# Performance work log

Measured on AMD Instinct MI355X. Metric: run time of the kernel, lower is better.

The kernel has to match this reference:

```python
import jax, jax.numpy as jnp
import numpy as np

ROPE_THETA = 10000.0

def rope(x):
    # RoPE over the FULL model_dim (applied pre head-split, as in the source),
    # interleaved even/odd pairs. x: [B, S, D]
    B, S, D = x.shape
    half = D // 2
    inv_freq = 1.0 / (ROPE_THETA ** (jnp.arange(half, dtype=jnp.float32) * 2.0 / D))
    ang = jnp.arange(S, dtype=jnp.float32)[:, None] * inv_freq[None, :]  # [S, half]
    cos, sin = jnp.cos(ang), jnp.sin(ang)
    x1, x2 = x[..., 0::2], x[..., 1::2]
    r1 = x1 * cos - x2 * sin
    r2 = x1 * sin + x2 * cos
    return jnp.stack([r1, r2], axis=-1).reshape(B, S, D)


def setup_inputs() -> dict:
    key = jax.random.key(0)
    ks = jax.random.split(key, 9)
    B, S, D = 4, 2048, 768
    w = 0.02
    return {
        "X":  jax.random.normal(ks[0], (B, S, D), dtype=jnp.float32),
        "Wq": jax.random.normal(ks[1], (D, D), dtype=jnp.float32) * w,
        "bq": jnp.zeros((D,), dtype=jnp.float32),
        "Wk": jax.random.normal(ks[2], (D, D), dtype=jnp.float32) * w,
        "bk": jnp.zeros((D,), dtype=jnp.float32),
        "Wv": jax.random.normal(ks[3], (D, D), dtype=jnp.float32) * w,
        "bv": jnp.zeros((D,), dtype=jnp.float32),
        "Wo": jax.random.normal(ks[4], (D, D), dtype=jnp.float32) * w,
        "bo": jnp.zeros((D,), dtype=jnp.float32),
    }


def reference(X, Wq, bq, Wk, bk, Wv, bv, Wo, bo):
    NUM_HEADS = 12
    B, S, D = X.shape
    hd = D // NUM_HEADS

    q = rope(X @ Wq + bq)   # RoPE applied pre-split on full model_dim
    k = rope(X @ Wk + bk)
    v = X @ Wv + bv

    # Contiguous per-head slices == reshape to [B, S, H, hd]
    qh = q.reshape(B, S, NUM_HEADS, hd)
    kh = k.reshape(B, S, NUM_HEADS, hd)
    vh = v.reshape(B, S, NUM_HEADS, hd)

    scores = jnp.einsum('bqhd,bkhd->bhqk', qh, kh) / jnp.sqrt(jnp.float32(hd))
    causal = jnp.tril(jnp.ones((S, S), dtype=bool))
    scores = jnp.where(causal[None, None, :, :], scores, -jnp.inf)
    weights = jax.nn.softmax(scores, axis=-1)
    out = jnp.einsum('bhqk,bkhd->bqhd', weights, vh).reshape(B, S, D)
    return out @ Wo + bo
```

## Files before the change

kernel.cpp:

```cpp
#include <hip/hip_runtime.h>
#include <math.h>

#define D_MODEL 768
#define NUM_HEADS 12
#define HEAD_DIM 64
#define SEQ 2048
#define BATCH 4
#define MROWS (BATCH * SEQ)
#define HALF_D (D_MODEL / 2)

typedef __bf16    bf16x8 __attribute__((ext_vector_type(8)));
typedef _Float16  f16x4  __attribute__((ext_vector_type(4)));
typedef float     f32x4  __attribute__((ext_vector_type(4)));

__device__ __forceinline__ void gload_lds16(const void* gp, void* lp) {
    __builtin_amdgcn_global_load_lds(
        (const __attribute__((address_space(1))) unsigned int*)gp,
        (__attribute__((address_space(3))) unsigned int*)lp, 16, 0, 0);
}

__global__ __launch_bounds__(256)
void prep(const float* __restrict__ X, __bf16* __restrict__ Xb,
          const float* __restrict__ W0, const float* __restrict__ W1,
          const float* __restrict__ W2, const float* __restrict__ W3,
          __bf16* __restrict__ T0, __bf16* __restrict__ T1,
          __bf16* __restrict__ T2, __bf16* __restrict__ T3)
{
    __shared__ float t[64][65];
    const int n   = blockIdx.x;
    const int tid = threadIdx.x;

    if (n < 3072) {
        size_t i = ((size_t)n * 256 + tid) * 8;
        float4 u = *(const float4*)(X + i);
        float4 v = *(const float4*)(X + i + 4);
        bf16x8 o;
        o[0]=(__bf16)u.x; o[1]=(__bf16)u.y; o[2]=(__bf16)u.z; o[3]=(__bf16)u.w;
        o[4]=(__bf16)v.x; o[5]=(__bf16)v.y; o[6]=(__bf16)v.z; o[7]=(__bf16)v.w;
        *(bf16x8*)(Xb + i) = o;
    } else {
        int m = n - 3072;
        int z = m / 144;
        int rem = m - z * 144;
        int by = rem / 12, bx = rem % 12;
        const float* W = z == 0 ? W0 : z == 1 ? W1 : z == 2 ? W2 : W3;
        __bf16*      T = z == 0 ? T0 : z == 1 ? T1 : z == 2 ? T2 : T3;

        const int r0 = by * 64, c0 = bx * 64;
        const int lx = tid & 63, g = tid >> 6;

        #pragma unroll
        for (int rr = 0; rr < 16; ++rr) {
            int r = g * 16 + rr;
            t[r][lx] = W[(size_t)(r0 + r) * D_MODEL + c0 + lx];
        }
        __syncthreads();

        const int nn = tid >> 2;
        const int kb = (tid & 3) * 16;
        bf16x8 o1, o2;
        #pragma unroll
        for (int mm = 0; mm < 8; ++mm) o1[mm] = (__bf16)t[kb + mm][nn];
        #pragma unroll
        for (int mm = 0; mm < 8; ++mm) o2[mm] = (__bf16)t[kb + 8 + mm][nn];
        __bf16* dst = T + (size_t)(c0 + nn) * D_MODEL + r0 + kb;
        *(bf16x8*)dst       = o1;
        *(bf16x8*)(dst + 8) = o2;
    }
}

__global__ __launch_bounds__(256)
void qkv_gemm(const __bf16* __restrict__ Xb,
              const __bf16* __restrict__ Wqt, const __bf16* __restrict__ Wkt,
              const __bf16* __restrict__ Wvt,
              const float* __restrict__ bq, const float* __restrict__ bk,
              const float* __restrict__ bv,
              __bf16* __restrict__ Qb, __bf16* __restrict__ Kb,
              _Float16* __restrict__ Vtb)
{
    __shared__ bf16x8 Asf[2][8][64];
    __shared__ bf16x8 Bsf[2][8][64];

    const int tid  = threadIdx.x;
    const int wv   = tid >> 6;
    const int ln   = tid & 63;
    const int t15  = ln & 15;
    const int quad = ln >> 4;
    const int wr = wv >> 1, wc = wv & 1;

    const int lin = blockIdx.x;
    const int c   = lin >> 6;
    const int r   = lin & 63;
    const int which = c / 6;
    const int col0  = (c % 6) * 128;
    const int row0  = r * 128;

    const __bf16* Wt  = which == 0 ? Wqt : which == 1 ? Wkt : Wvt;
    const float* bias = which == 0 ? bq  : which == 1 ? bk  : bv;

    f32x4 acc[4][4];
    #pragma unroll
    for (int i = 0; i < 4; ++i)
        #pragma unroll
        for (int j = 0; j < 4; ++j) acc[i][j] = (f32x4){0.f,0.f,0.f,0.f};

    const __bf16* a0 = Xb + (size_t)(row0 + 16 * wv       + t15) * D_MODEL + 8 * quad;
    const __bf16* a1 = Xb + (size_t)(row0 + 16 * (wv + 4) + t15) * D_MODEL + 8 * quad;
    const __bf16* b0 = Wt + (size_t)(col0 + 16 * wv       + t15) * D_MODEL + 8 * quad;
    const __bf16* b1 = Wt + (size_t)(col0 + 16 * (wv + 4) + t15) * D_MODEL + 8 * quad;

    for (int k0 = 0; k0 < D_MODEL; k0 += 64) {
        __syncthreads();
        #pragma unroll
        for (int ks = 0; ks < 2; ++ks) {
            const int kk = k0 + 32 * ks;
            gload_lds16(a0 + kk, &Asf[ks][wv][0]);
            gload_lds16(a1 + kk, &Asf[ks][wv + 4][0]);
            gload_lds16(b0 + kk, &Bsf[ks][wv][0]);
            gload_lds16(b1 + kk, &Bsf[ks][wv + 4][0]);
        }
        __syncthreads();

        #pragma unroll
        for (int ks = 0; ks < 2; ++ks) {
            bf16x8 af[4], bfr[4];
            #pragma unroll
            for (int i = 0; i < 4; ++i) af[i]  = Asf[ks][4 * wr + i][ln];
            #pragma unroll
            for (int j = 0; j < 4; ++j) bfr[j] = Bsf[ks][4 * wc + j][ln];
            #pragma unroll
            for (int i = 0; i < 4; ++i)
                #pragma unroll
                for (int j = 0; j < 4; ++j)
                    acc[i][j] = __builtin_amdgcn_mfma_f32_16x16x32_bf16(af[i], bfr[j], acc[i][j], 0, 0, 0);
        }
    }

    #pragma unroll
    for (int i = 0; i < 4; ++i) {
        const int rowb = row0 + 64 * wr + 16 * i + 4 * quad;
        #pragma unroll
        for (int j = 0; j < 4; ++j) {
            const int col = col0 + 64 * wc + 16 * j + t15;
            const float bval = bias[col];
            if (which < 2) {
                const int ne = col & ~1;
                const float fr = __expf((float)ne * (-9.210340371976184f / 768.0f));
                const float cf = __cosf(fr), sf = __sinf(fr);
                const float sgn = (col & 1) ? 1.0f : -1.0f;
                const float oscale = (which == 0) ? 0.125f : 1.0f;
                __bf16* dst = (which ? Kb : Qb);
                const int s0 = rowb & (SEQ - 1);
                float ang = (float)s0 * fr;
                float ca = __cosf(ang), sa = __sinf(ang);
                #pragma unroll
                for (int rr = 0; rr < 4; ++rr) {
                    const int rw = rowb + rr;
                    float val  = acc[i][j][rr] + bval;
                    float part = __shfl_xor(val, 1, 64);
                    dst[(size_t)rw * D_MODEL + col] = (__bf16)((val * ca + part * sgn * sa) * oscale);
                    float cn = ca * cf - sa * sf;
                    sa = sa * cf + ca * sf;
                    ca = cn;
                }
            } else {
                const int h = col >> 6, d = col & 63;
                const int bidx = rowb >> 11, s = rowb & (SEQ - 1);
                f16x4 pk;
                #pragma unroll
                for (int rr = 0; rr < 4; ++rr) pk[rr] = (_Float16)(acc[i][j][rr] + bval);
                *(f16x4*)(Vtb + ((size_t)(bidx * NUM_HEADS + h) * 64 + d) * SEQ + s) = pk;
            }
        }
    }
}

__global__ __launch_bounds__(256)
void out_gemm(const __bf16* __restrict__ Ab, const __bf16* __restrict__ Wt,
              const float* __restrict__ bias, float* __restrict__ Cout)
{
    __shared__ bf16x8 Asf[2][4][64];
    __shared__ bf16x8 Bsf[2][8][64];

    const int tid  = threadIdx.x;
    const int wv   = tid >> 6;
    const int ln   = tid & 63;
    const int t15  = ln & 15;
    const int quad = ln >> 4;
    const int wr = wv >> 1, wc = wv & 1;

    const int lin  = blockIdx.x;
    const int col0 = (lin >> 7) * 128;
    const int row0 = (lin & 127) * 64;

    f32x4 acc[2][4];
    #pragma unroll
    for (int i = 0; i < 2; ++i)
        #pragma unroll
        for (int j = 0; j < 4; ++j) acc[i][j] = (f32x4){0.f,0.f,0.f,0.f};

    for (int k0 = 0; k0 < D_MODEL; k0 += 64) {
        __syncthreads();
        #pragma unroll
        for (int u = 0; u < 6; ++u) {
            const int id = wv * 6 + u;
            const int ks = id / 12;
            const int w  = id % 12;
            if (w < 4) {
                const __bf16* src = Ab + (size_t)(row0 + 16 * w + t15) * D_MODEL
                                       + k0 + 32 * ks + 8 * quad;
                gload_lds16(src, &Asf[ks][w][0]);
            } else {
                const __bf16* src = Wt + (size_t)(col0 + 16 * (w - 4) + t15) * D_MODEL
                                       + k0 + 32 * ks + 8 * quad;
                gload_lds16(src, &Bsf[ks][w - 4][0]);
            }
        }
        __syncthreads();

        #pragma unroll
        for (int ks = 0; ks < 2; ++ks) {
            bf16x8 af[2], bfr[4];
            #pragma unroll
            for (int i = 0; i < 2; ++i) af[i]  = Asf[ks][2 * wr + i][ln];
            #pragma unroll
            for (int j = 0; j < 4; ++j) bfr[j] = Bsf[ks][4 * wc + j][ln];
            #pragma unroll
            for (int i = 0; i < 2; ++i)
                #pragma unroll
                for (int j = 0; j < 4; ++j)
                    acc[i][j] = __builtin_amdgcn_mfma_f32_16x16x32_bf16(af[i], bfr[j], acc[i][j], 0, 0, 0);
        }
    }

    #pragma unroll
    for (int i = 0; i < 2; ++i) {
        const int rowb = row0 + 32 * wr + 16 * i + 4 * quad;
        #pragma unroll
        for (int j = 0; j < 4; ++j) {
            const int col = col0 + 64 * wc + 16 * j + t15;
            const float bval = bias[col];
            #pragma unroll
            for (int rr = 0; rr < 4; ++rr)
                Cout[(size_t)(rowb + rr) * D_MODEL + col] = acc[i][j][rr] + bval;
        }
    }
}

__device__ __forceinline__ void attn_tile(
    const bf16x8 (*Kbuf)[64], const _Float16* Vbuf ,
    bf16x8 aq0, bf16x8 aq1,
    f32x4* o, float& lacc,
    int ln, int t15, int quad, int j0, int qglob, bool domask)
{
    f32x4 s[4];
    #pragma unroll
    for (int c = 0; c < 4; ++c) {
        s[c] = (f32x4){0.f, 0.f, 0.f, 0.f};
        s[c] = __builtin_amdgcn_mfma_f32_16x16x32_bf16(Kbuf[c][ln],     aq0, s[c], 0, 0, 0);
        s[c] = __builtin_amdgcn_mfma_f32_16x16x32_bf16(Kbuf[4 + c][ln], aq1, s[c], 0, 0, 0);
    }

    f16x4 pf[4];
    #pragma unroll
    for (int c = 0; c < 4; ++c)
        #pragma unroll
        for (int r = 0; r < 4; ++r) {
            float e = __expf(s[c][r]);
            if (domask && (j0 + 16 * c + 4 * quad + r > qglob)) e = 0.f;
            lacc += e;
            pf[c][r] = (_Float16)e;
        }

    #pragma unroll
    for (int c = 0; c < 4; ++c) {
        const int lv = 16 * (2 * (c & 1) + (quad >> 1)) + t15;
        const int jb = 4 * (quad & 1);
        #pragma unroll
        for (int cd = 0; cd < 4; ++cd) {
            f16x4 vf = *(const f16x4*)&Vbuf[(size_t)(4 * (c >> 1) + cd) * 512 + lv * 8 + jb];
            o[cd] = __builtin_amdgcn_mfma_f32_16x16x16f16(pf[c], vf, o[cd], 0, 0, 0);
        }
    }
}

__global__ __launch_bounds__(512)
void attn_flash(const __bf16* __restrict__ Q, const __bf16* __restrict__ K,
                const _Float16* __restrict__ Vt, __bf16* __restrict__ O)
{
    __shared__ bf16x8   Kf[2][8][64];
    __shared__ _Float16 Vh[2][8][512];

    const int tid  = threadIdx.x;
    const int wv   = tid >> 6;
    const int ln   = tid & 63;
    const int t15  = ln & 15;
    const int quad = ln >> 4;

    const int n  = blockIdx.x;
    const int qt = 15 - (n / 48);
    const int bh = n % 48;
    const int b  = bh / NUM_HEADS;
    const int h  = bh % NUM_HEADS;
    const int q0 = qt * 128;
    const int nt = (q0 >> 6) + 2;

    bf16x8 aq0, aq1;
    {
        const __bf16* qs = Q + (size_t)(b * SEQ + q0 + 16 * wv + t15) * D_MODEL + h * 64 + 8 * quad;
        aq0 = *(const bf16x8*)qs;
        aq1 = *(const bf16x8*)(qs + 32);
    }

    const __bf16*   kp = K  + ((size_t)b * SEQ + 16 * (wv & 3) + t15) * D_MODEL
                            + h * 64 + 32 * (wv >> 2) + 8 * quad;
    const _Float16* vp = Vt + ((size_t)bh * 64 + 16 * (wv & 3) + t15) * SEQ
                            + 32 * (wv >> 2) + 8 * quad;

    f32x4 o[4];
    #pragma unroll
    for (int c = 0; c < 4; ++c) o[c] = (f32x4){0.f,0.f,0.f,0.f};
    float lacc = 0.f;
    const int qglob = q0 + 16 * wv + t15;
    const int wmax  = q0 + 16 * wv + 15;

    gload_lds16(kp, &Kf[0][wv][0]);
    gload_lds16(vp, &Vh[0][wv][0]);

    int cur = 0;
    for (int it = 0; it < nt; ++it) {
        __syncthreads();
        if (it + 1 < nt) {
            const int jn = (it + 1) * 64;
            gload_lds16(kp + (size_t)jn * D_MODEL, &Kf[cur ^ 1][wv][0]);
            gload_lds16(vp + jn,                   &Vh[cur ^ 1][wv][0]);
        }
        const int j0 = it * 64;
        if (j0 <= wmax) {
            const bool domask = (j0 + 63) > (q0 + 16 * wv);
            attn_tile(Kf[cur], &Vh[cur][0][0], aq0, aq1, o, lacc,
                      ln, t15, quad, j0, qglob, domask);
        }
        cur ^= 1;
    }

    lacc += __shfl_xor(lacc, 16, 64);
    lacc += __shfl_xor(lacc, 32, 64);

    float inv[4];
    #pragma unroll
    for (int r = 0; r < 4; ++r)
        inv[r] = 1.0f / __shfl(lacc, 4 * quad + r, 64);

    #pragma unroll
    for (int c = 0; c < 4; ++c)
        #pragma unroll
        for (int r = 0; r < 4; ++r) {
            int row = q0 + 16 * wv + 4 * quad + r;
            O[(size_t)(b * SEQ + row) * D_MODEL + h * 64 + 16 * c + t15] = (__bf16)(o[c][r] * inv[r]);
        }
}

extern "C" void kernel_launch(void* const* d_in, const int* in_sizes, int n_in,
                              void* d_out, int out_size, void* d_ws, size_t ws_size,
                              hipStream_t stream) {
    const float* X  = (const float*)d_in[0];
    const float* Wq = (const float*)d_in[1];
    const float* bq = (const float*)d_in[2];
    const float* Wk = (const float*)d_in[3];
    const float* bk = (const float*)d_in[4];
    const float* Wv = (const float*)d_in[5];
    const float* bv = (const float*)d_in[6];
    const float* Wo = (const float*)d_in[7];
    const float* bo = (const float*)d_in[8];
    float* out = (float*)d_out;

    const size_t BSD = (size_t)MROWS * D_MODEL;
    const size_t WSZ = (size_t)D_MODEL * D_MODEL;

    __bf16*   Xb  = (__bf16*)d_ws;
    __bf16*   Qb  = Xb  + BSD;
    __bf16*   Kb  = Qb  + BSD;
    _Float16* Vtb = (_Float16*)(Kb + BSD);
    __bf16*   Ob  = (__bf16*)(Vtb + BSD);
    __bf16*   Wqt = Ob  + BSD;
    __bf16*   Wkt = Wqt + WSZ;
    __bf16*   Wvt = Wkt + WSZ;
    __bf16*   Wot = Wvt + WSZ;

    prep<<<3648, 256, 0, stream>>>(X, Xb, Wq, Wk, Wv, Wo, Wqt, Wkt, Wvt, Wot);

    qkv_gemm<<<1152, 256, 0, stream>>>(Xb, Wqt, Wkt, Wvt, bq, bk, bv, Qb, Kb, Vtb);

    attn_flash<<<768, 512, 0, stream>>>(Qb, Kb, Vtb, Ob);

    out_gemm<<<768, 256, 0, stream>>>(Ob, Wot, bo, out);
}
```

Before: 243.5 us.

## Double-buffer LDS in projection GEMMs and precompute RoPE cos/sin table

```diff
diff --git a/kernel.cpp b/kernel.cpp
--- a/kernel.cpp
+++ b/kernel.cpp
@@ -24,7 +24,8 @@
           const float* __restrict__ W0, const float* __restrict__ W1,
           const float* __restrict__ W2, const float* __restrict__ W3,
           __bf16* __restrict__ T0, __bf16* __restrict__ T1,
-          __bf16* __restrict__ T2, __bf16* __restrict__ T3)
+          __bf16* __restrict__ T2, __bf16* __restrict__ T3,
+          float2* __restrict__ Rt)
 {
     __shared__ float t[64][65];
     const int n   = blockIdx.x;
@@ -38,7 +39,7 @@
         o[0]=(__bf16)u.x; o[1]=(__bf16)u.y; o[2]=(__bf16)u.z; o[3]=(__bf16)u.w;
         o[4]=(__bf16)v.x; o[5]=(__bf16)v.y; o[6]=(__bf16)v.z; o[7]=(__bf16)v.w;
         *(bf16x8*)(Xb + i) = o;
-    } else {
+    } else if (n < 3648) {
         int m = n - 3072;
         int z = m / 144;
         int rem = m - z * 144;
@@ -66,6 +67,26 @@
         __bf16* dst = T + (size_t)(c0 + nn) * D_MODEL + r0 + kb;
         *(bf16x8*)dst       = o1;
         *(bf16x8*)(dst + 8) = o2;
+    } else {
+        const int m = n - 3648;
+        const int e = (m * 256 + tid) * 4;
+        const int s  = e / HALF_D;
+        const int f0 = e - s * HALF_D;
+        const float fs = (float)s;
+        float c[4], sv[4];
+        #pragma unroll
+        for (int u = 0; u < 4; ++u) {
+            float fr = __expf((float)(2 * (f0 + u)) * (-9.210340371976184f / 768.0f));
+            float ang = fs * fr;
+            c[u]  = __cosf(ang);
+            sv[u] = __sinf(ang);
+        }
+        float* dstp = (float*)(Rt + e);
+        float4 o01, o23;
+        o01.x = c[0]; o01.y = sv[0]; o01.z = c[1]; o01.w = sv[1];
+        o23.x = c[2]; o23.y = sv[2]; o23.z = c[3]; o23.w = sv[3];
+        *(float4*)dstp       = o01;
+        *(float4*)(dstp + 4) = o23;
     }
 }
 
@@ -75,11 +96,12 @@
               const __bf16* __restrict__ Wvt,
               const float* __restrict__ bq, const float* __restrict__ bk,
               const float* __restrict__ bv,
+              const float2* __restrict__ Rt,
               __bf16* __restrict__ Qb, __bf16* __restrict__ Kb,
               _Float16* __restrict__ Vtb)
 {
-    __shared__ bf16x8 Asf[2][8][64];
-    __shared__ bf16x8 Bsf[2][8][64];
+    __shared__ bf16x8 Asf[2][2][8][64];
+    __shared__ bf16x8 Bsf[2][2][8][64];
 
     const int tid  = threadIdx.x;
     const int wv   = tid >> 6;
@@ -109,61 +131,73 @@
     const __bf16* b0 = Wt + (size_t)(col0 + 16 * wv       + t15) * D_MODEL + 8 * quad;
     const __bf16* b1 = Wt + (size_t)(col0 + 16 * (wv + 4) + t15) * D_MODEL + 8 * quad;
 
-    for (int k0 = 0; k0 < D_MODEL; k0 += 64) {
-        __syncthreads();
+    auto stage = [&](int buf, int k0) {
         #pragma unroll
         for (int ks = 0; ks < 2; ++ks) {
             const int kk = k0 + 32 * ks;
-            gload_lds16(a0 + kk, &Asf[ks][wv][0]);
-            gload_lds16(a1 + kk, &Asf[ks][wv + 4][0]);
-            gload_lds16(b0 + kk, &Bsf[ks][wv][0]);
-            gload_lds16(b1 + kk, &Bsf[ks][wv + 4][0]);
-        }
-        __syncthreads();
+            gload_lds16(a0 + kk, &Asf[buf][ks][wv][0]);
+            gload_lds16(a1 + kk, &Asf[buf][ks][wv + 4][0]);
+            gload_lds16(b0 + kk, &Bsf[buf][ks][wv][0]);
+            gload_lds16(b1 + kk, &Bsf[buf][ks][wv + 4][0]);
+        }
+    };
+
+    stage(0, 0);
+    __syncthreads();
+
+    int cur = 0;
+    for (int k0 = 0; k0 < D_MODEL; k0 += 64) {
+        if (k0 + 64 < D_MODEL)
+            stage(cur ^ 1, k0 + 64);
 
         #pragma unroll
         for (int ks = 0; ks < 2; ++ks) {
             bf16x8 af[4], bfr[4];
             #pragma unroll
-            for (int i = 0; i < 4; ++i) af[i]  = Asf[ks][4 * wr + i][ln];
-            #pragma unroll
-            for (int j = 0; j < 4; ++j) bfr[j] = Bsf[ks][4 * wc + j][ln];
+            for (int i = 0; i < 4; ++i) af[i]  = Asf[cur][ks][4 * wr + i][ln];
+            #pragma unroll
+            for (int j = 0; j < 4; ++j) bfr[j] = Bsf[cur][ks][4 * wc + j][ln];
             #pragma unroll
             for (int i = 0; i < 4; ++i)
                 #pragma unroll
                 for (int j = 0; j < 4; ++j)
                     acc[i][j] = __builtin_amdgcn_mfma_f32_16x16x32_bf16(af[i], bfr[j], acc[i][j], 0, 0, 0);
         }
-    }
-
-    #pragma unroll
-    for (int i = 0; i < 4; ++i) {
-        const int rowb = row0 + 64 * wr + 16 * i + 4 * quad;
-        #pragma unroll
-        for (int j = 0; j < 4; ++j) {
-            const int col = col0 + 64 * wc + 16 * j + t15;
-            const float bval = bias[col];
-            if (which < 2) {
-                const int ne = col & ~1;
-                const float fr = __expf((float)ne * (-9.210340371976184f / 768.0f));
-                const float cf = __cosf(fr), sf = __sinf(fr);
-                const float sgn = (col & 1) ? 1.0f : -1.0f;
-                const float oscale = (which == 0) ? 0.125f : 1.0f;
-                __bf16* dst = (which ? Kb : Qb);
-                const int s0 = rowb & (SEQ - 1);
-                float ang = (float)s0 * fr;
-                float ca = __cosf(ang), sa = __sinf(ang);
+        __syncthreads();
+        cur ^= 1;
+    }
+
+    if (which < 2) {
+        const float oscale = (which == 0) ? 0.125f : 1.0f;
+        __bf16* dst = which ? Kb : Qb;
+        #pragma unroll
+        for (int i = 0; i < 4; ++i) {
+            const int rowb = row0 + 64 * wr + 16 * i + 4 * quad;
+            const int s0   = rowb & (SEQ - 1);
+            #pragma unroll
+            for (int j = 0; j < 4; ++j) {
+                const int col = col0 + 64 * wc + 16 * j + t15;
+                const float bval = bias[col];
+                const float sgn  = (col & 1) ? 1.0f : -1.0f;
+                const int   f    = col >> 1;
                 #pragma unroll
                 for (int rr = 0; rr < 4; ++rr) {
-                    const int rw = rowb + rr;
+                    float2 cs = Rt[(size_t)(s0 + rr) * HALF_D + f];
                     float val  = acc[i][j][rr] + bval;
                     float part = __shfl_xor(val, 1, 64);
-                    dst[(size_t)rw * D_MODEL + col] = (__bf16)((val * ca + part * sgn * sa) * oscale);
-                    float cn = ca * cf - sa * sf;
-                    sa = sa * cf + ca * sf;
-                    ca = cn;
+                    dst[(size_t)(rowb + rr) * D_MODEL + col] =
+                        (__bf16)((val * cs.x + part * sgn * cs.y) * oscale);
                 }
-            } else {
+            }
+        }
+    } else {
+        #pragma unroll
+        for (int i = 0; i < 4; ++i) {
+            const int rowb = row0 + 64 * wr + 16 * i + 4 * quad;
+            #pragma unroll
+            for (int j = 0; j < 4; ++j) {
+                const int col = col0 + 64 * wc + 16 * j + t15;
+                const float bval = bias[col];
                 const int h = col >> 6, d = col & 63;
                 const int bidx = rowb >> 11, s = rowb & (SEQ - 1);
                 f16x4 pk;
@@ -179,8 +213,8 @@
 void out_gemm(const __bf16* __restrict__ Ab, const __bf16* __restrict__ Wt,
               const float* __restrict__ bias, float* __restrict__ Cout)
 {
-    __shared__ bf16x8 Asf[2][4][64];
-    __shared__ bf16x8 Bsf[2][8][64];
+    __shared__ bf16x8 Asf[2][2][4][64];
+    __shared__ bf16x8 Bsf[2][2][8][64];
 
     const int tid  = threadIdx.x;
     const int wv   = tid >> 6;
@@ -199,8 +233,7 @@
         #pragma unroll
         for (int j = 0; j < 4; ++j) acc[i][j] = (f32x4){0.f,0.f,0.f,0.f};
 
-    for (int k0 = 0; k0 < D_MODEL; k0 += 64) {
-        __syncthreads();
+    auto stage = [&](int buf, int k0) {
         #pragma unroll
         for (int u = 0; u < 6; ++u) {
             const int id = wv * 6 + u;
@@ -209,28 +242,38 @@
             if (w < 4) {
                 const __bf16* src = Ab + (size_t)(row0 + 16 * w + t15) * D_MODEL
                                        + k0 + 32 * ks + 8 * quad;
-                gload_lds16(src, &Asf[ks][w][0]);
+                gload_lds16(src, &Asf[buf][ks][w][0]);
             } else {
                 const __bf16* src = Wt + (size_t)(col0 + 16 * (w - 4) + t15) * D_MODEL
                                        + k0 + 32 * ks + 8 * quad;
-                gload_lds16(src, &Bsf[ks][w - 4][0]);
+                gload_lds16(src, &Bsf[buf][ks][w - 4][0]);
             }
         }
-        __syncthreads();
+    };
+
+    stage(0, 0);
+    __syncthreads();
+
+    int cur = 0;
+    for (int k0 = 0; k0 < D_MODEL; k0 += 64) {
+        if (k0 + 64 < D_MODEL)
+            stage(cur ^ 1, k0 + 64);
 
         #pragma unroll
         for (int ks = 0; ks < 2; ++ks) {
             bf16x8 af[2], bfr[4];
             #pragma unroll
-            for (int i = 0; i < 2; ++i) af[i]  = Asf[ks][2 * wr + i][ln];
-            #pragma unroll
-            for (int j = 0; j < 4; ++j) bfr[j] = Bsf[ks][4 * wc + j][ln];
+            for (int i = 0; i < 2; ++i) af[i]  = Asf[cur][ks][2 * wr + i][ln];
+            #pragma unroll
+            for (int j = 0; j < 4; ++j) bfr[j] = Bsf[cur][ks][4 * wc + j][ln];
             #pragma unroll
             for (int i = 0; i < 2; ++i)
                 #pragma unroll
                 for (int j = 0; j < 4; ++j)
                     acc[i][j] = __builtin_amdgcn_mfma_f32_16x16x32_bf16(af[i], bfr[j], acc[i][j], 0, 0, 0);
         }
+        __syncthreads();
+        cur ^= 1;
     }
 
     #pragma unroll
@@ -387,10 +430,11 @@
     __bf16*   Wkt = Wqt + WSZ;
     __bf16*   Wvt = Wkt + WSZ;
     __bf16*   Wot = Wvt + WSZ;
-
-    prep<<<3648, 256, 0, stream>>>(X, Xb, Wq, Wk, Wv, Wo, Wqt, Wkt, Wvt, Wot);
-
-    qkv_gemm<<<1152, 256, 0, stream>>>(Xb, Wqt, Wkt, Wvt, bq, bk, bv, Qb, Kb, Vtb);
+    float2*   Rt  = (float2*)(Wot + WSZ);
+
+    prep<<<4416, 256, 0, stream>>>(X, Xb, Wq, Wk, Wv, Wo, Wqt, Wkt, Wvt, Wot, Rt);
+
+    qkv_gemm<<<1152, 256, 0, stream>>>(Xb, Wqt, Wkt, Wvt, bq, bk, bv, Rt, Qb, Kb, Vtb);
 
     attn_flash<<<768, 512, 0, stream>>>(Qb, Kb, Vtb, Ob);
 
```

Result: slower. 259.4 us (+6.5%).
